# Kernel optimization log

Hardware: AMD Instinct MI355X
Metric: run time of the kernel (lower is better)

The kernel has to match this reference:

```python
import jax, jax.numpy as jnp
import numpy as np

N_IMG, N_CAP, N_RGN, MAX_W, EMBED = 32, 32, 36, 50, 1024
LAMBDA_SOFTMAX = 9.0
NORM_EPS = 1e-12  # F.normalize default eps


def setup_inputs() -> dict:
    key = jax.random.key(0)
    ks = jax.random.split(key, 13)
    rgn = jax.random.normal(ks[0], (N_IMG, N_RGN, EMBED), jnp.float32)
    img = jax.random.normal(ks[1], (N_IMG, EMBED), jnp.float32)
    wrd = jax.random.normal(ks[2], (N_CAP, MAX_W, EMBED), jnp.float32)
    stc = jax.random.normal(ks[3], (N_CAP, EMBED), jnp.float32)
    # ragged caption lengths in [1, MAX_W]
    stc_lens = jax.random.randint(ks[4], (N_CAP,), 1, MAX_W + 1, dtype=jnp.int32)
    s = 1.0 / np.sqrt(EMBED)
    w_scale = jax.random.normal(ks[5], (EMBED, EMBED), jnp.float32) * s
    b_scale = jnp.zeros((EMBED,), jnp.float32)
    w_shift = jax.random.normal(ks[6], (EMBED, EMBED), jnp.float32) * s
    b_shift = jnp.zeros((EMBED,), jnp.float32)
    w1 = jax.random.normal(ks[7], (EMBED, EMBED), jnp.float32) * s
    b1 = jnp.zeros((EMBED,), jnp.float32)
    w2 = jax.random.normal(ks[8], (EMBED, EMBED), jnp.float32) * s
    b2 = jnp.zeros((EMBED,), jnp.float32)
    return dict(rgn=rgn, img=img, wrd=wrd, stc=stc, stc_lens=stc_lens,
                w_scale=w_scale, b_scale=b_scale, w_shift=w_shift, b_shift=b_shift,
                w1=w1, b1=b1, w2=w2, b2=b2)


def reference(rgn, img, wrd, stc, stc_lens, w_scale, b_scale, w_shift, b_shift, w1, b1, w2, b2):
    # rgn: (I, Q, D) regions; wrd: (C, L, D) ragged words; stc_lens: (C,)
    C, L, D = wrd.shape
    valid = jnp.arange(L)[None, :] < stc_lens[:, None]          # (C, L)
    # scores[c,i,l,q] = wrd[c,l] . rgn[i,q]  (bmm(context, queryT))
    s = jnp.einsum('cld,iqd->cilq', wrd, rgn)                   # (C, I, L, Q)
    s = jnp.where(s >= 0, s, 0.1 * s)                           # LeakyReLU(0.1)
    # L2-normalize over the query (region) axis, per (c,i,l)
    s = s / jnp.maximum(jnp.sqrt(jnp.sum(s * s, axis=3, keepdims=True)), NORM_EPS)
    # temperature softmax over valid words (ragged mask)
    logits = jnp.where(valid[:, None, :, None], s * LAMBDA_SOFTMAX, -jnp.inf)
    attn = jax.nn.softmax(logits, axis=2)                       # (C, I, L, Q)
    # weightedContext[c,i,q,d] = sum_l attn * wrd
    wei = jnp.einsum('cilq,cld->ciqd', attn, wrd)               # (C, I, Q, D)
    # FiLM-style refine
    scaling = jnp.tanh(jnp.einsum('ciqd,ed->ciqe', wei, w_scale) + b_scale)
    shifting = jnp.einsum('ciqd,ed->ciqe', wei, w_shift) + b_shift
    x = rgn[None] * scaling + shifting                          # (C, I, Q, D)
    h = jax.nn.relu(jnp.einsum('ciqd,ed->ciqe', x, w1) + b1)
    modu = jnp.einsum('ciqd,ed->ciqe', h, w2) + b2
    ref = modu + rgn[None]
    # torch cats per-caption results along dim=1 -> (I, C, Q, D)
    return jnp.transpose(ref, (1, 0, 2, 3))
```

## Files before the change

### kernel.cpp

```cpp
#include <hip/hip_runtime.h>
#include <math.h>

#define NC 32
#define NI 32
#define NL 50
#define NQ 36
#define ND 1024
#define LAMBDA 9.0f

#define BM 128
#define BN 128
#define BK 32

typedef __attribute__((ext_vector_type(8))) short bf16x8;
typedef __attribute__((ext_vector_type(4))) float floatx4;

static __device__ __forceinline__ unsigned short f2b(float f) {
    unsigned int u = __float_as_uint(f);
    unsigned int r = (u + 0x7fffu + ((u >> 16) & 1u)) >> 16;
    return (unsigned short)r;
}
static __device__ __forceinline__ float bf2f(unsigned short u) {
    return __uint_as_float(((unsigned int)u) << 16);
}

static __device__ __forceinline__ float ftanh(float x) {
    float ax = fabsf(x);
    float e = __expf(ax + ax);
    return copysignf(1.f - 2.f / (e + 1.f), x);
}

static __device__ __forceinline__ void gload16(const unsigned short* g, unsigned short* l) {
    __builtin_amdgcn_global_load_lds(
        (const __attribute__((address_space(1))) unsigned int*)g,
        (__attribute__((address_space(3))) unsigned int*)l, 16, 0, 0);
}

struct CvtJob { const float* src; unsigned short* dst; int n2; int valid2; };
struct CvtJobs { CvtJob j[5]; };

__global__ __launch_bounds__(256) void k_cvt(CvtJobs jobs) {
    CvtJob jb = jobs.j[blockIdx.y];
    unsigned int* d32 = (unsigned int*)jb.dst;
    int stride = gridDim.x * 256;
    for (int i = blockIdx.x * 256 + threadIdx.x; i < jb.n2; i += stride) {
        unsigned int pk = 0;
        if (i < jb.valid2) {
            float2 v = ((const float2*)jb.src)[i];
            pk = (unsigned int)f2b(v.x) | ((unsigned int)f2b(v.y) << 16);
        }
        d32[i] = pk;
    }
}

struct HlJob { const float* src; unsigned short* hi; unsigned short* lo; int n2; };
struct HlJobs { HlJob j[2]; };

__global__ __launch_bounds__(256) void k_cvt_hilo(HlJobs jobs) {
    HlJob jb = jobs.j[blockIdx.y];
    unsigned int* h32 = (unsigned int*)jb.hi;
    unsigned int* l32 = (unsigned int*)jb.lo;
    int stride = gridDim.x * 256;
    for (int i = blockIdx.x * 256 + threadIdx.x; i < jb.n2; i += stride) {
        float2 v = ((const float2*)jb.src)[i];
        unsigned short h0 = f2b(v.x), h1 = f2b(v.y);
        unsigned short l0 = f2b(v.x - bf2f(h0)), l1 = f2b(v.y - bf2f(h1));
        h32[i] = (unsigned int)h0 | ((unsigned int)h1 << 16);
        l32[i] = (unsigned int)l0 | ((unsigned int)l1 << 16);
    }
}

#define SST 37

__global__ __launch_bounds__(256) void k_attn(
    const unsigned short* __restrict__ whi, const unsigned short* __restrict__ wlo,
    const unsigned short* __restrict__ rhi, const unsigned short* __restrict__ rlo,
    const int* __restrict__ lens, unsigned short* __restrict__ attn)
{
    int bx = blockIdx.x;
    int c = bx / NI, i = bx % NI;
    __shared__ __align__(16) unsigned short Wh[64 * 32], Wl[64 * 32];
    __shared__ __align__(16) unsigned short Rh[48 * 32], Rl[48 * 32];
    __shared__ float S[64 * SST];
    int t = threadIdx.x, lane = t & 63, wid = t >> 6;
    int lrow = lane & 15, quad = lane >> 4;
    int len = lens[c];

    int grow = lane >> 2;
    int ssw = ((lane & 3) ^ ((lane >> 3) & 3)) * 8;
    const unsigned short* garr = (wid == 0) ? whi : (wid == 1) ? wlo : (wid == 2) ? rhi : rlo;
    unsigned short* larr = (wid == 0) ? Wh : (wid == 1) ? Wl : (wid == 2) ? Rh : Rl;
    int ngroups = (wid < 2) ? 4 : 3;
    size_t gbase = (wid < 2) ? (size_t)(c * NL) * ND : (size_t)(i * NQ) * ND;

    floatx4 acc[3] = {};
    int fsw = (quad ^ ((lrow >> 1) & 3)) * 8;

    for (int kt = 0; kt < ND; kt += 32) {
        for (int j = 0; j < ngroups; ++j) {
            int row = j * 16 + grow;
            gload16(garr + gbase + (size_t)row * ND + kt + ssw, larr + j * 512 + lane * 8);
        }
        __syncthreads();
        bf16x8 ah = *(const bf16x8*)&Wh[(wid * 16 + lrow) * 32 + fsw];
        bf16x8 al = *(const bf16x8*)&Wl[(wid * 16 + lrow) * 32 + fsw];
#pragma unroll
        for (int nt = 0; nt < 3; ++nt) {
            bf16x8 bh = *(const bf16x8*)&Rh[(nt * 16 + lrow) * 32 + fsw];
            bf16x8 bl = *(const bf16x8*)&Rl[(nt * 16 + lrow) * 32 + fsw];
            acc[nt] = __builtin_amdgcn_mfma_f32_16x16x32_bf16(ah, bh, acc[nt], 0, 0, 0);
            acc[nt] = __builtin_amdgcn_mfma_f32_16x16x32_bf16(ah, bl, acc[nt], 0, 0, 0);
            acc[nt] = __builtin_amdgcn_mfma_f32_16x16x32_bf16(al, bh, acc[nt], 0, 0, 0);
        }
        __syncthreads();
    }
#pragma unroll
    for (int nt = 0; nt < 3; ++nt) {
        int q = nt * 16 + lrow;
        if (q < NQ) {
#pragma unroll
            for (int r = 0; r < 4; ++r) {
                int l = wid * 16 + quad * 4 + r;
                S[l * SST + q] = acc[nt][r];
            }
        }
    }
    __syncthreads();
    if (t < 200) {
        int l = t >> 2, part = t & 3;
        float lv[9];
        float ss = 0.f;
#pragma unroll
        for (int jj = 0; jj < 9; ++jj) {
            int q = part * 9 + jj;
            float v = S[l * SST + q];
            float x = (v >= 0.f) ? v : 0.1f * v;
            lv[jj] = x;
            ss += x * x;
        }
        ss += __shfl_xor(ss, 1);
        ss += __shfl_xor(ss, 2);
        float inv = LAMBDA / fmaxf(sqrtf(ss), 1e-12f);
#pragma unroll
        for (int jj = 0; jj < 9; ++jj) S[l * SST + part * 9 + jj] = lv[jj] * inv;
    }
    __syncthreads();
    if (t < 144) {
        int q = t >> 2, part = t & 3;
        int ls = part * 13;
        int le = ls + 13 < len ? ls + 13 : len;
        float m = -1e30f;
        for (int l = ls; l < le; ++l) m = fmaxf(m, S[l * SST + q]);
        m = fmaxf(m, __shfl_xor(m, 1));
        m = fmaxf(m, __shfl_xor(m, 2));
        float sum = 0.f;
        for (int l = ls; l < le; ++l) sum += __expf(S[l * SST + q] - m);
        sum += __shfl_xor(sum, 1);
        sum += __shfl_xor(sum, 2);
        float inv = 1.f / sum;
        unsigned int* o = (unsigned int*)attn + ((size_t)(c * NI + i) * NQ + q) * 32;
        int jb = part * 8;
#pragma unroll
        for (int jj = 0; jj < 8; ++jj) {
            int j = jb + jj;
            int l0 = 2 * j, l1 = 2 * j + 1;
            unsigned short a0 = (l0 < len) ? f2b(__expf(S[l0 * SST + q] - m) * inv) : (unsigned short)0;
            unsigned short a1 = (l1 < len) ? f2b(__expf(S[l1 * SST + q] - m) * inv) : (unsigned short)0;
            o[j] = (unsigned int)a0 | ((unsigned int)a1 << 16);
        }
    }
}

__global__ __launch_bounds__(256, 2) void k_pgemm(
    const unsigned short* __restrict__ A, const unsigned short* __restrict__ B1,
    const unsigned short* __restrict__ B2, unsigned short* __restrict__ P1,
    unsigned short* __restrict__ P2)
{
    const int K = ND;
    int bn = blockIdx.x, bm = blockIdx.y;
    const unsigned short* B = blockIdx.z ? B2 : B1;
    unsigned short* P = blockIdx.z ? P2 : P1;
    int m0 = bm * BM, n0 = bn * BN;

    __shared__ __align__(16) unsigned short At[BM * BK];
    __shared__ __align__(16) unsigned short Bt[BN * BK];

    int t = threadIdx.x, lane = t & 63, wid = t >> 6;
    int wx = wid & 1, wy = wid >> 1;
    int lrow = lane & 15, quad = lane >> 4;
    floatx4 acc[4][4] = {};

    int srow = t >> 2, pos = t & 3;
    int ssw = (pos ^ ((srow >> 1) & 3)) * 8;
    const unsigned short* Aptr = A + (size_t)(m0 + srow) * K + ssw;
    const unsigned short* Bptr = B + (size_t)(n0 + srow) * K + ssw;
    unsigned short* Al  = &At[srow * BK + pos * 8];
    unsigned short* Al2 = &At[(srow + 64) * BK + pos * 8];
    unsigned short* Bl  = &Bt[srow * BK + pos * 8];
    unsigned short* Bl2 = &Bt[(srow + 64) * BK + pos * 8];
    int fsw = (quad ^ ((lrow >> 1) & 3)) * 8;

    for (int kt = 0; kt < K; kt += BK) {
        gload16(Aptr + kt, Al);
        gload16(Aptr + (size_t)64 * K + kt, Al2);
        gload16(Bptr + kt, Bl);
        gload16(Bptr + (size_t)64 * K + kt, Bl2);
        __syncthreads();
        bf16x8 af[4], bfr[4];
#pragma unroll
        for (int im = 0; im < 4; ++im)
            af[im] = *(const bf16x8*)&At[(wy * 64 + im * 16 + lrow) * BK + fsw];
#pragma unroll
        for (int in = 0; in < 4; ++in)
            bfr[in] = *(const bf16x8*)&Bt[(wx * 64 + in * 16 + lrow) * BK + fsw];
#pragma unroll
        for (int im = 0; im < 4; ++im)
#pragma unroll
            for (int in = 0; in < 4; ++in)
                acc[im][in] = __builtin_amdgcn_mfma_f32_16x16x32_bf16(
                    af[im], bfr[in], acc[im][in], 0, 0, 0);
        __syncthreads();
    }
#pragma unroll
    for (int im = 0; im < 4; ++im)
#pragma unroll
        for (int in = 0; in < 4; ++in) {
            int n = n0 + wx * 64 + in * 16 + lrow;
#pragma unroll
            for (int r = 0; r < 4; ++r) {
                int m = m0 + wy * 64 + im * 16 + quad * 4 + r;
                int c = m / NL, l = m - c * NL;
                if (c < NC) P[((size_t)(c * ND + n)) * 64 + l] = f2b(acc[im][in][r]);
            }
        }
}

__global__ __launch_bounds__(256, 2) void k_attn_gemm(
    const unsigned short* __restrict__ attn, const unsigned short* __restrict__ Psc,
    const unsigned short* __restrict__ Psh, const float* __restrict__ bsc,
    const float* __restrict__ bsh, const float* __restrict__ rgnf,
    unsigned short* __restrict__ xbuf)
{
    int bn = blockIdx.x, bm = blockIdx.y, c = blockIdx.z;
    __shared__ __align__(16) unsigned short At[128 * 64], B1t[128 * 64], B2t[128 * 64];
    int t = threadIdx.x, lane = t & 63, wid = t >> 6;
    int wx = wid & 1, wy = wid >> 1;
    int lrow = lane & 15, quad = lane >> 4;
    int grow = lane >> 3, pos = lane & 7;

    const unsigned short* Ab  = attn + (size_t)(c * 1152 + bm * 128) * 64;
    const unsigned short* B1b = Psc + (size_t)(c * ND + bn * 128) * 64;
    const unsigned short* B2b = Psh + (size_t)(c * ND + bn * 128) * 64;
    for (int g = wid; g < 16; g += 4) {
        int row = g * 8 + grow;
        int ssw = (pos ^ (row & 7)) * 8;
        gload16(Ab + (size_t)row * 64 + ssw, &At[g * 512 + lane * 8]);
        gload16(B1b + (size_t)row * 64 + ssw, &B1t[g * 512 + lane * 8]);
        gload16(B2b + (size_t)row * 64 + ssw, &B2t[g * 512 + lane * 8]);
    }
    __syncthreads();

    floatx4 acc[4][4] = {}, acc2[4][4] = {};
#pragma unroll
    for (int kk = 0; kk < 2; ++kk) {
        int sw = ((kk * 4 + quad) ^ (lrow & 7)) * 8;
        bf16x8 af[4], b1f[4], b2f[4];
#pragma unroll
        for (int im = 0; im < 4; ++im)
            af[im] = *(const bf16x8*)&At[(wy * 64 + im * 16 + lrow) * 64 + sw];
#pragma unroll
        for (int in = 0; in < 4; ++in) {
            b1f[in] = *(const bf16x8*)&B1t[(wx * 64 + in * 16 + lrow) * 64 + sw];
            b2f[in] = *(const bf16x8*)&B2t[(wx * 64 + in * 16 + lrow) * 64 + sw];
        }
#pragma unroll
        for (int im = 0; im < 4; ++im)
#pragma unroll
            for (int in = 0; in < 4; ++in) {
                acc[im][in] = __builtin_amdgcn_mfma_f32_16x16x32_bf16(
                    af[im], b1f[in], acc[im][in], 0, 0, 0);
                acc2[im][in] = __builtin_amdgcn_mfma_f32_16x16x32_bf16(
                    af[im], b2f[in], acc2[im][in], 0, 0, 0);
            }
    }
#pragma unroll
    for (int im = 0; im < 4; ++im)
#pragma unroll
        for (int in = 0; in < 4; ++in) {
            int n = bn * 128 + wx * 64 + in * 16 + lrow;
            float b1v = bsc[n], b2v = bsh[n];
#pragma unroll
            for (int r = 0; r < 4; ++r) {
                int m = bm * 128 + wy * 64 + im * 16 + quad * 4 + r;
                int i = m / NQ, q = m - i * NQ;
                float sc = ftanh(acc[im][in][r] + b1v);
                float sh = acc2[im][in][r] + b2v;
                float rg = rgnf[(size_t)(i * NQ + q) * ND + n];
                xbuf[((size_t)(c * 1152 + m)) * ND + n] = f2b(rg * sc + sh);
            }
        }
}

template <int MODE, int MINW>
__global__ __launch_bounds__(256, MINW) void k_gemm(
    const unsigned short* __restrict__ A, const unsigned short* __restrict__ B1,
    const float* __restrict__ bias1, const float* __restrict__ rgnf,
    void* __restrict__ outp)
{
    const int K = ND;
    int lin = blockIdx.x;
    int xcd = lin & 7;
    int kb = lin >> 3;
    int bm = xcd * 36 + (kb >> 3);
    int bn = kb & 7;
    int m0 = bm * BM, n0 = bn * BN;

    __shared__ __align__(16) unsigned short At[BM * BK];
    __shared__ __align__(16) unsigned short Bt[BN * BK];

    int t = threadIdx.x;
    int lane = t & 63, wid = t >> 6;
    int wx = wid & 1, wy = wid >> 1;
    int lrow = lane & 15, quad = lane >> 4;

    floatx4 acc[4][4] = {};

    int srow = t >> 2, pos = t & 3;
    int ssw = (pos ^ ((srow >> 1) & 3)) * 8;
    const unsigned short* Aptr  = A  + (size_t)(m0 + srow) * K + ssw;
    const unsigned short* B1ptr = B1 + (size_t)(n0 + srow) * K + ssw;
    unsigned short* Al  = &At[srow * BK + pos * 8];
    unsigned short* Al2 = &At[(srow + 64) * BK + pos * 8];
    unsigned short* Bl  = &Bt[srow * BK + pos * 8];
    unsigned short* Bl2 = &Bt[(srow + 64) * BK + pos * 8];
    int fsw = (quad ^ ((lrow >> 1) & 3)) * 8;

    for (int kt = 0; kt < K; kt += BK) {
        gload16(Aptr + kt, Al);
        gload16(Aptr + (size_t)64 * K + kt, Al2);
        gload16(B1ptr + kt, Bl);
        gload16(B1ptr + (size_t)64 * K + kt, Bl2);
        __syncthreads();

        bf16x8 af[4], bfr[4];
#pragma unroll
        for (int im = 0; im < 4; ++im)
            af[im] = *(const bf16x8*)&At[(wy * 64 + im * 16 + lrow) * BK + fsw];
#pragma unroll
        for (int in = 0; in < 4; ++in)
            bfr[in] = *(const bf16x8*)&Bt[(wx * 64 + in * 16 + lrow) * BK + fsw];
#pragma unroll
        for (int im = 0; im < 4; ++im)
#pragma unroll
            for (int in = 0; in < 4; ++in)
                acc[im][in] = __builtin_amdgcn_mfma_f32_16x16x32_bf16(
                    af[im], bfr[in], acc[im][in], 0, 0, 0);
        __syncthreads();
    }

#pragma unroll
    for (int im = 0; im < 4; ++im) {
#pragma unroll
        for (int in = 0; in < 4; ++in) {
            int n = n0 + wx * 64 + in * 16 + lrow;
            float b1v = bias1[n];
#pragma unroll
            for (int r = 0; r < 4; ++r) {
                int m = m0 + wy * 64 + im * 16 + quad * 4 + r;
                int q = m % NQ;
                int ci = m / NQ;
                int i = ci % NI, c = ci / NI;
                float v = acc[im][in][r];
                if constexpr (MODE == 1) {
                    float h = v + b1v;
                    ((unsigned short*)outp)[(size_t)m * ND + n] = f2b(h > 0.f ? h : 0.f);
                } else {
                    float rg = rgnf[(size_t)(i * NQ + q) * ND + n];
                    ((float*)outp)[((size_t)(i * NC + c) * NQ + q) * ND + n] = v + b1v + rg;
                }
            }
        }
    }
}

extern "C" void kernel_launch(void* const* d_in, const int* in_sizes, int n_in,
                              void* d_out, int out_size, void* d_ws, size_t ws_size,
                              hipStream_t stream) {
    const float* rgn     = (const float*)d_in[0];
    const float* wrd     = (const float*)d_in[2];
    const int*   lens    = (const int*)d_in[4];
    const float* w_scale = (const float*)d_in[5];
    const float* b_scale = (const float*)d_in[6];
    const float* w_shift = (const float*)d_in[7];
    const float* b_shift = (const float*)d_in[8];
    const float* w1      = (const float*)d_in[9];
    const float* b1      = (const float*)d_in[10];
    const float* w2      = (const float*)d_in[11];
    const float* b2      = (const float*)d_in[12];
    float* outf = (float*)d_out;

    char* ws = (char*)d_ws;
    unsigned short* wsc_bf = (unsigned short*)(ws + 0);
    unsigned short* wsh_bf = (unsigned short*)(ws + 2097152);
    unsigned short* w1_bf  = (unsigned short*)(ws + 4194304);
    unsigned short* w2_bf  = (unsigned short*)(ws + 6291456);
    unsigned short* wrd_bf = (unsigned short*)(ws + 8388608);
    unsigned short* attn   = (unsigned short*)(ws + 11796480);
    unsigned short* P_sct  = (unsigned short*)(ws + 16515072);
    unsigned short* P_sht  = (unsigned short*)(ws + 20709376);
    unsigned short* wrd_hi = (unsigned short*)(ws + 24903680);
    unsigned short* wrd_lo = (unsigned short*)(ws + 28209152);
    unsigned short* rgn_hi = (unsigned short*)(ws + 31514624);
    unsigned short* rgn_lo = (unsigned short*)(ws + 33898496);
    unsigned short* hbuf   = (unsigned short*)(ws + 8388608);
    unsigned short* xbuf   = (unsigned short*)d_out;

    CvtJobs jobs;
    jobs.j[0] = { w_scale, wsc_bf, ND * ND / 2, ND * ND / 2 };
    jobs.j[1] = { w_shift, wsh_bf, ND * ND / 2, ND * ND / 2 };
    jobs.j[2] = { w1,      w1_bf,  ND * ND / 2, ND * ND / 2 };
    jobs.j[3] = { w2,      w2_bf,  ND * ND / 2, ND * ND / 2 };
    jobs.j[4] = { wrd,     wrd_bf, 1664 * ND / 2, NC * NL * ND / 2 };
    k_cvt<<<dim3(128, 5), 256, 0, stream>>>(jobs);

    HlJobs hjobs;
    hjobs.j[0] = { wrd, wrd_hi, wrd_lo, NC * NL * ND / 2 };
    hjobs.j[1] = { rgn, rgn_hi, rgn_lo, NI * NQ * ND / 2 };
    k_cvt_hilo<<<dim3(128, 2), 256, 0, stream>>>(hjobs);

    k_attn<<<NC * NI, 256, 0, stream>>>(wrd_hi, wrd_lo, rgn_hi, rgn_lo, lens, attn);

    k_pgemm<<<dim3(8, 13, 2), 256, 0, stream>>>(wrd_bf, wsc_bf, wsh_bf, P_sct, P_sht);

    k_attn_gemm<<<dim3(8, 9, 32), 256, 0, stream>>>(attn, P_sct, P_sht,
                                                    b_scale, b_shift, rgn, xbuf);

    k_gemm<1, 2><<<2304, 256, 0, stream>>>(xbuf, w1_bf, b1, rgn, hbuf);
    k_gemm<2, 2><<<2304, 256, 0, stream>>>(hbuf, w2_bf, b2, rgn, outf);
}
```

Before: 493.3 us.

## Stage GEMM epilogues through LDS, double BK, and reorder xbuf to output layout

The attention-GEMM and MLP-GEMM epilogues now write results into a swizzled LDS tile, then store 16-byte vectors to global memory instead of scattered 2-byte stores. xbuf is laid out in (image, caption, region) row order, so the final GEMM can write the transposed output contiguously without per-element index remapping. The main GEMM K-tile grows from 32 to 64 with a new XOR swizzle, halving the number of sync barriers per tile. This costs more LDS per block and extra barriers in the epilogue, which could reduce occupancy.

```diff
diff --git a/kernel.cpp b/kernel.cpp
--- a/kernel.cpp
+++ b/kernel.cpp
@@ -10,7 +10,6 @@
 
 #define BM 128
 #define BN 128
-#define BK 32
 
 typedef __attribute__((ext_vector_type(8))) short bf16x8;
 typedef __attribute__((ext_vector_type(4))) float floatx4;
@@ -177,13 +176,14 @@
     unsigned short* __restrict__ P2)
 {
     const int K = ND;
+    const int BK = 32;
     int bn = blockIdx.x, bm = blockIdx.y;
     const unsigned short* B = blockIdx.z ? B2 : B1;
     unsigned short* P = blockIdx.z ? P2 : P1;
     int m0 = bm * BM, n0 = bn * BN;
 
-    __shared__ __align__(16) unsigned short At[BM * BK];
-    __shared__ __align__(16) unsigned short Bt[BN * BK];
+    __shared__ __align__(16) unsigned short At[BM * 32];
+    __shared__ __align__(16) unsigned short Bt[BN * 32];
 
     int t = threadIdx.x, lane = t & 63, wid = t >> 6;
     int wx = wid & 1, wy = wid >> 1;
@@ -242,7 +242,11 @@
     unsigned short* __restrict__ xbuf)
 {
     int bn = blockIdx.x, bm = blockIdx.y, c = blockIdx.z;
-    __shared__ __align__(16) unsigned short At[128 * 64], B1t[128 * 64], B2t[128 * 64];
+    __shared__ __align__(16) unsigned short smem3[3 * 128 * 64];
+    unsigned short* At  = smem3;
+    unsigned short* B1t = smem3 + 8192;
+    unsigned short* B2t = smem3 + 16384;
+    unsigned short* Ct  = smem3;
     int t = threadIdx.x, lane = t & 63, wid = t >> 6;
     int wx = wid & 1, wy = wid >> 1;
     int lrow = lane & 15, quad = lane >> 4;
@@ -283,6 +287,7 @@
                     af[im], b2f[in], acc2[im][in], 0, 0, 0);
             }
     }
+    __syncthreads();
 #pragma unroll
     for (int im = 0; im < 4; ++im)
 #pragma unroll
@@ -291,14 +296,25 @@
             float b1v = bsc[n], b2v = bsh[n];
 #pragma unroll
             for (int r = 0; r < 4; ++r) {
-                int m = bm * 128 + wy * 64 + im * 16 + quad * 4 + r;
+                int row = wy * 64 + im * 16 + quad * 4 + r;
+                int m = bm * 128 + row;
                 int i = m / NQ, q = m - i * NQ;
                 float sc = ftanh(acc[im][in][r] + b1v);
                 float sh = acc2[im][in][r] + b2v;
                 float rg = rgnf[(size_t)(i * NQ + q) * ND + n];
-                xbuf[((size_t)(c * 1152 + m)) * ND + n] = f2b(rg * sc + sh);
-            }
-        }
+                int colc = (wx * 8 + in * 2 + (lrow >> 3)) ^ (row & 7);
+                Ct[row * 128 + colc * 8 + (lrow & 7)] = f2b(rg * sc + sh);
+            }
+        }
+    __syncthreads();
+#pragma unroll
+    for (int p = 0; p < 8; ++p) {
+        int row = p * 16 + (t >> 4), chunk = t & 15;
+        int m = bm * 128 + row;
+        int i = m / NQ, q = m - i * NQ;
+        size_t dr = ((size_t)(i * NC + c) * NQ + q) * ND + bn * 128 + chunk * 8;
+        *(bf16x8*)&xbuf[dr] = *(const bf16x8*)&Ct[row * 128 + ((chunk ^ (row & 7)) * 8)];
+    }
 }
 
 template <int MODE, int MINW>
@@ -315,8 +331,10 @@
     int bn = kb & 7;
     int m0 = bm * BM, n0 = bn * BN;
 
-    __shared__ __align__(16) unsigned short At[BM * BK];
-    __shared__ __align__(16) unsigned short Bt[BN * BK];
+    __shared__ __align__(16) unsigned short smem[2 * 128 * 64];
+    unsigned short* At = smem;
+    unsigned short* Bt = smem + 8192;
+    unsigned short* Ct = smem;
 
     int t = threadIdx.x;
     int lane = t & 63, wid = t >> 6;
@@ -325,61 +343,80 @@
 
     floatx4 acc[4][4] = {};
 
-    int srow = t >> 2, pos = t & 3;
-    int ssw = (pos ^ ((srow >> 1) & 3)) * 8;
+    int srow = t >> 3, pos = t & 7;
+    int ssw = (pos ^ (srow & 7)) * 8;
     const unsigned short* Aptr  = A  + (size_t)(m0 + srow) * K + ssw;
     const unsigned short* B1ptr = B1 + (size_t)(n0 + srow) * K + ssw;
-    unsigned short* Al  = &At[srow * BK + pos * 8];
-    unsigned short* Al2 = &At[(srow + 64) * BK + pos * 8];
-    unsigned short* Bl  = &Bt[srow * BK + pos * 8];
-    unsigned short* Bl2 = &Bt[(srow + 64) * BK + pos * 8];
-    int fsw = (quad ^ ((lrow >> 1) & 3)) * 8;
-
-    for (int kt = 0; kt < K; kt += BK) {
-        gload16(Aptr + kt, Al);
-        gload16(Aptr + (size_t)64 * K + kt, Al2);
-        gload16(B1ptr + kt, Bl);
-        gload16(B1ptr + (size_t)64 * K + kt, Bl2);
-        __syncthreads();
-
-        bf16x8 af[4], bfr[4];
-#pragma unroll
-        for (int im = 0; im < 4; ++im)
-            af[im] = *(const bf16x8*)&At[(wy * 64 + im * 16 + lrow) * BK + fsw];
-#pragma unroll
-        for (int in = 0; in < 4; ++in)
-            bfr[in] = *(const bf16x8*)&Bt[(wx * 64 + in * 16 + lrow) * BK + fsw];
-#pragma unroll
-        for (int im = 0; im < 4; ++im)
+    unsigned short* ldA = At + t * 8;
+    unsigned short* ldB = Bt + t * 8;
+
+    for (int kt = 0; kt < K; kt += 64) {
+#pragma unroll
+        for (int p = 0; p < 4; ++p) {
+            gload16(Aptr + (size_t)(p * 32) * K + kt, ldA + p * 2048);
+            gload16(B1ptr + (size_t)(p * 32) * K + kt, ldB + p * 2048);
+        }
+        __syncthreads();
+#pragma unroll
+        for (int kh = 0; kh < 2; ++kh) {
+            int sw = ((kh * 4 + quad) ^ (lrow & 7)) * 8;
+            bf16x8 af[4], bfr[4];
+#pragma unroll
+            for (int im = 0; im < 4; ++im)
+                af[im] = *(const bf16x8*)&At[(wy * 64 + im * 16 + lrow) * 64 + sw];
 #pragma unroll
             for (int in = 0; in < 4; ++in)
-                acc[im][in] = __builtin_amdgcn_mfma_f32_16x16x32_bf16(
-                    af[im], bfr[in], acc[im][in], 0, 0, 0);
-        __syncthreads();
-    }
-
-#pragma unroll
-    for (int im = 0; im < 4; ++im) {
-#pragma unroll
-        for (int in = 0; in < 4; ++in) {
-            int n = n0 + wx * 64 + in * 16 + lrow;
-            float b1v = bias1[n];
-#pragma unroll
-            for (int r = 0; r < 4; ++r) {
-                int m = m0 + wy * 64 + im * 16 + quad * 4 + r;
-                int q = m % NQ;
-                int ci = m / NQ;
-                int i = ci % NI, c = ci / NI;
-                float v = acc[im][in][r];
-                if constexpr (MODE == 1) {
-                    float h = v + b1v;
-                    ((unsigned short*)outp)[(size_t)m * ND + n] = f2b(h > 0.f ? h : 0.f);
-                } else {
+                bfr[in] = *(const bf16x8*)&Bt[(wx * 64 + in * 16 + lrow) * 64 + sw];
+#pragma unroll
+            for (int im = 0; im < 4; ++im)
+#pragma unroll
+                for (int in = 0; in < 4; ++in)
+                    acc[im][in] = __builtin_amdgcn_mfma_f32_16x16x32_bf16(
+                        af[im], bfr[in], acc[im][in], 0, 0, 0);
+        }
+        __syncthreads();
+    }
+
+    if constexpr (MODE == 1) {
+#pragma unroll
+        for (int im = 0; im < 4; ++im)
+#pragma unroll
+            for (int in = 0; in < 4; ++in) {
+                int n = n0 + wx * 64 + in * 16 + lrow;
+                float b1v = bias1[n];
+#pragma unroll
+                for (int r = 0; r < 4; ++r) {
+                    int row = wy * 64 + im * 16 + quad * 4 + r;
+                    float h = acc[im][in][r] + b1v;
+                    h = h > 0.f ? h : 0.f;
+                    int colc = (wx * 8 + in * 2 + (lrow >> 3)) ^ (row & 7);
+                    Ct[row * 128 + colc * 8 + (lrow & 7)] = f2b(h);
+                }
+            }
+        __syncthreads();
+        unsigned short* ob = (unsigned short*)outp + (size_t)m0 * ND + n0;
+#pragma unroll
+        for (int p = 0; p < 8; ++p) {
+            int row = p * 16 + (t >> 4), chunk = t & 15;
+            *(bf16x8*)&ob[(size_t)row * ND + chunk * 8] =
+                *(const bf16x8*)&Ct[row * 128 + ((chunk ^ (row & 7)) * 8)];
+        }
+    } else {
+#pragma unroll
+        for (int im = 0; im < 4; ++im)
+#pragma unroll
+            for (int in = 0; in < 4; ++in) {
+                int n = n0 + wx * 64 + in * 16 + lrow;
+                float b1v = bias1[n];
+#pragma unroll
+                for (int r = 0; r < 4; ++r) {
+                    int m = m0 + wy * 64 + im * 16 + quad * 4 + r;
+                    int i = m / (NC * NQ);
+                    int q = m % NQ;
                     float rg = rgnf[(size_t)(i * NQ + q) * ND + n];
-                    ((float*)outp)[((size_t)(i * NC + c) * NQ + q) * ND + n] = v + b1v + rg;
+                    ((float*)outp)[(size_t)m * ND + n] = acc[im][in][r] + b1v + rg;
                 }
             }
-        }
     }
 }
 
```

Result: faster. 435.5 us (-11.7%).
